# Kernel tuning notes

Hardware: AMD Instinct MI355X
Metric: run time of the kernel (lower is better)

Reference implementation:

```python
import jax, jax.numpy as jnp
import numpy as np

B, T, D, H = 32, 2048, 256, 512


def setup_inputs() -> dict:
    key = jax.random.key(0)
    k1, k2, k3, k4 = jax.random.split(key, 4)
    datamat = jax.random.normal(k1, (B, T, D), jnp.float32)
    datalens = jax.random.randint(k2, (B,), 0, T, jnp.int32)
    si = 1.0 / np.sqrt(D)
    sh = 1.0 / np.sqrt(H)
    # flax OptimizedLSTMCell: input dense has no bias, hidden dense has bias.
    Wi = jax.random.uniform(k3, (D, 4 * H), jnp.float32, -si, si)
    Wh = jax.random.uniform(k4, (H, 4 * H), jnp.float32, -sh, sh)
    b = jnp.zeros((4 * H,), jnp.float32)
    return {"datamat": datamat, "datalens": datalens, "Wi": Wi, "Wh": Wh, "b": b}


def _lstm(datamat, datalens, Wi, Wh, b):
    Bsz, Tlen, _ = datamat.shape
    Hd = Wh.shape[0]
    # Precompute input projection for all timesteps: [B,T,4H]
    x_proj = jnp.einsum('btd,dg->btg', datamat, Wi)
    c0 = jnp.zeros((Bsz, Hd), datamat.dtype)
    h0 = jnp.zeros((Bsz, Hd), datamat.dtype)

    def step(state, xg):
        c, h, lc, lh, t = state
        gates = xg + h @ Wh + b            # [B,4H], gate order i,f,g,o
        i, f, g, o = jnp.split(gates, 4, axis=-1)
        new_c = jax.nn.sigmoid(f) * c + jax.nn.sigmoid(i) * jnp.tanh(g)
        new_h = jax.nn.sigmoid(o) * jnp.tanh(new_c)
        # latch carry at the last valid step (t < seq_len), matching flax RNN
        # which selects the carry at index seq_len-1 from an unmasked scan.
        valid = (t < datalens)[:, None]
        lc = jnp.where(valid, new_c, lc)
        lh = jnp.where(valid, new_h, lh)
        return (new_c, new_h, lc, lh, t + 1), new_h

    init = (c0, h0, c0, h0, jnp.int32(0))
    (_, _, lc, lh, _), ys = jax.lax.scan(step, init, jnp.swapaxes(x_proj, 0, 1))
    return (lc, lh), jnp.swapaxes(ys, 0, 1)  # carry=(c,h), outputs [B,T,H]


def reference(datamat, datalens, Wi, Wh, b):
    return _lstm(datamat, datalens, Wi, Wh, b)
```

## Files before the change

kernel.cpp:

```cpp
#include <hip/hip_runtime.h>
#include <cstdint>

static constexpr int BATCH  = 32;
static constexpr int TLEN   = 2048;
static constexpr int DIN    = 256;
static constexpr int HDIM   = 512;
static constexpr int G4     = 2048;
static constexpr int NSLICE = 8;
static constexpr int HCB    = 64;
static constexpr int CPB    = 256;
static constexpr int NTHR   = 512;
static constexpr int NWAVE  = 8;
static constexpr int KL     = 96;
static constexpr int KL2    = 48;
static constexpr int NBLK   = BATCH * NSLICE;

typedef _Float16 h2v __attribute__((ext_vector_type(2)));
typedef uint32_t u32x4 __attribute__((ext_vector_type(4)));

__device__ __forceinline__ uint32_t pack_f16x2(float a, float b) {
    h2v v;
    v[0] = (_Float16)a;
    v[1] = (_Float16)b;
    return __builtin_bit_cast(uint32_t, v);
}

__device__ __forceinline__ float dot2f(uint32_t w, uint32_t u, float acc) {
#if __has_builtin(__builtin_amdgcn_fdot2)
    return __builtin_amdgcn_fdot2(__builtin_bit_cast(h2v, w),
                                  __builtin_bit_cast(h2v, u), acc, false);
#else
    h2v a = __builtin_bit_cast(h2v, w);
    h2v b = __builtin_bit_cast(h2v, u);
    return acc + (float)a[0] * (float)b[0] + (float)a[1] * (float)b[1];
#endif
}

__device__ __forceinline__ float sigmoidf_(float x) {
    return 1.0f / (1.0f + __expf(-x));
}
__device__ __forceinline__ float tanhf_(float x) {
    return 1.0f - 2.0f / (1.0f + __expf(2.0f * x));
}

__device__ __forceinline__ u32x4 load_agent_u128(const uint32_t* p) {
    u32x4 r;
    asm volatile("global_load_dwordx4 %0, %1, off sc0 sc1\n\t"
                 "s_waitcnt vmcnt(0)"
                 : "=&v"(r) : "v"(p) : "memory");
    return r;
}

__global__ __launch_bounds__(NTHR, 2)
__attribute__((amdgpu_waves_per_eu(2, 2)))
void lstm_persist(
    const float* __restrict__ x, const int* __restrict__ lens,
    const float* __restrict__ Wi, const float* __restrict__ Wh,
    const float* __restrict__ bias, float* __restrict__ out,
    uint32_t* __restrict__ hT)
{
    const int bid = blockIdx.x;
    const int xcd = bid & 7;
    const int t8  = bid >> 3;
    const int b   = xcd * 4 + (t8 & 3);
    const int s   = t8 >> 2;

    const int tid = threadIdx.x;
    const int w   = tid >> 6;
    const int l   = tid & 63;

    __shared__ __align__(16) uint32_t u_lds[NWAVE][KL2];
    __shared__ float gp[2][NWAVE][CPB];

    uint32_t wgt[4][KL2];
    #pragma unroll
    for (int q = 0; q < 4; ++q) {
        const int c    = 4 * l + q;
        const int gcol = (c >> 6) * HDIM + s * HCB + (c & 63);
        #pragma unroll
        for (int m = 0; m < KL2; ++m) {
            const int k0 = KL * w + 2 * m;
            const int k1 = k0 + 1;
            const float f0 = (k0 < DIN) ? Wi[(size_t)k0 * G4 + gcol]
                                        : Wh[(size_t)(k0 - DIN) * G4 + gcol];
            const float f1 = (k1 < DIN) ? Wi[(size_t)k1 * G4 + gcol]
                                        : Wh[(size_t)(k1 - DIN) * G4 + gcol];
            wgt[q][m] = pack_f16x2(f0, f1);
        }
    }

    float c_st = 0.f, lc_st = 0.f, lh_st = 0.f;
    float b_i = 0.f, b_f = 0.f, b_g = 0.f, b_o = 0.f;
    if (tid < HCB) {
        const int col = s * HCB + tid;
        b_i = bias[col];
        b_f = bias[HDIM + col];
        b_g = bias[2 * HDIM + col];
        b_o = bias[3 * HDIM + col];
    }
    const int len_b = lens[b];

    const float* xb = x + (size_t)b * TLEN * DIN;
    float* ys = out + 2 * BATCH * HDIM;

    const int  k0    = KL * w + 2 * l;
    const int  hk0   = KL * w + 4 * l;
    const bool is_x  = (l < KL2) && (k0 < DIN);
    const bool is_h4 = (l < KL2 / 2) && (hk0 >= DIN);

    float2 xx_cur = make_float2(0.f, 0.f);
    if (is_x) xx_cur = *(const float2*)(xb + k0);

    for (int t = 0; t < TLEN; ++t) {
        if (is_x) {
            u_lds[w][l] = pack_f16x2(xx_cur.x, xx_cur.y);
            if (t + 1 < TLEN)
                xx_cur = *(const float2*)(xb + (size_t)(t + 1) * DIN + k0);
        }
        if (is_h4) {
            const uint32_t* src =
                hT + (((size_t)(t & 1) * BATCH + b) * HDIM + (hk0 - DIN));
            const uint32_t tag = (uint32_t)t;
            u32x4 v;
            for (;;) {
                v = load_agent_u128(src);
                if ((v.x >> 16) == tag && (v.y >> 16) == tag &&
                    (v.z >> 16) == tag && (v.w >> 16) == tag) break;
            }
            uint2 pr;
            pr.x = (v.x & 0xFFFFu) | (v.y << 16);
            pr.y = (v.z & 0xFFFFu) | (v.w << 16);
            *(uint2*)&u_lds[w][2 * l] = pr;
        }

        float a0 = 0.f, a1 = 0.f, a2 = 0.f, a3 = 0.f;
        const uint4* uv = (const uint4*)&u_lds[w][0];
        #pragma unroll
        for (int m4 = 0; m4 < KL2 / 4; ++m4) {
            const uint4 uu = uv[m4];
            a0 = dot2f(wgt[0][4 * m4 + 0], uu.x, a0);
            a0 = dot2f(wgt[0][4 * m4 + 1], uu.y, a0);
            a0 = dot2f(wgt[0][4 * m4 + 2], uu.z, a0);
            a0 = dot2f(wgt[0][4 * m4 + 3], uu.w, a0);
            a1 = dot2f(wgt[1][4 * m4 + 0], uu.x, a1);
            a1 = dot2f(wgt[1][4 * m4 + 1], uu.y, a1);
            a1 = dot2f(wgt[1][4 * m4 + 2], uu.z, a1);
            a1 = dot2f(wgt[1][4 * m4 + 3], uu.w, a1);
            a2 = dot2f(wgt[2][4 * m4 + 0], uu.x, a2);
            a2 = dot2f(wgt[2][4 * m4 + 1], uu.y, a2);
            a2 = dot2f(wgt[2][4 * m4 + 2], uu.z, a2);
            a2 = dot2f(wgt[2][4 * m4 + 3], uu.w, a2);
            a3 = dot2f(wgt[3][4 * m4 + 0], uu.x, a3);
            a3 = dot2f(wgt[3][4 * m4 + 1], uu.y, a3);
            a3 = dot2f(wgt[3][4 * m4 + 2], uu.z, a3);
            a3 = dot2f(wgt[3][4 * m4 + 3], uu.w, a3);
        }
        float4 av;
        av.x = a0; av.y = a1; av.z = a2; av.w = a3;
        *(float4*)&gp[t & 1][w][4 * l] = av;

        __syncthreads();

        if (tid < HCB) {
            float si = b_i, sf = b_f, sg = b_g, so = b_o;
            #pragma unroll
            for (int ww = 0; ww < NWAVE; ++ww) {
                si += gp[t & 1][ww][tid];
                sf += gp[t & 1][ww][HCB + tid];
                sg += gp[t & 1][ww][2 * HCB + tid];
                so += gp[t & 1][ww][3 * HCB + tid];
            }
            const float ig = sigmoidf_(si);
            const float fg = sigmoidf_(sf);
            const float gg = tanhf_(sg);
            const float og = sigmoidf_(so);
            const float cn = fg * c_st + ig * gg;
            const float hn = og * tanhf_(cn);
            c_st = cn;
            if (t < len_b) { lc_st = cn; lh_st = hn; }
            const _Float16 hf = (_Float16)hn;
            const uint32_t word = ((uint32_t)(t + 1) << 16) |
                                  (uint32_t)__builtin_bit_cast(uint16_t, hf);
            __hip_atomic_store(
                &hT[((size_t)((t + 1) & 1) * BATCH + b) * HDIM + s * HCB + tid],
                word, __ATOMIC_RELAXED, __HIP_MEMORY_SCOPE_AGENT);
            ys[((size_t)b * TLEN + t) * HDIM + s * HCB + tid] = hn;
        }
    }

    if (tid < HCB) {
        out[(size_t)b * HDIM + s * HCB + tid] = lc_st;
        out[BATCH * HDIM + (size_t)b * HDIM + s * HCB + tid] = lh_st;
    }
}

extern "C" void kernel_launch(void* const* d_in, const int* in_sizes, int n_in,
                              void* d_out, int out_size, void* d_ws, size_t ws_size,
                              hipStream_t stream)
{
    const float* x    = (const float*)d_in[0];
    const int*   lens = (const int*)d_in[1];
    const float* Wi   = (const float*)d_in[2];
    const float* Wh   = (const float*)d_in[3];
    const float* bias = (const float*)d_in[4];
    float* out = (float*)d_out;

    uint32_t* hT = (uint32_t*)d_ws;
    const size_t init_bytes = (size_t)2 * BATCH * HDIM * sizeof(uint32_t);
    hipMemsetAsync(d_ws, 0, init_bytes, stream);

    hipLaunchKernelGGL(lstm_persist, dim3(NBLK), dim3(NTHR), 0, stream,
                       x, lens, Wi, Wh, bias, out, hT);
}
```

Before: 4.009 ms.

## Poll hidden state with a single wave and broadcast via LDS flag

Instead of several waves each spin-polling a slice of the previous hidden state from global memory, wave 7 alone polls the full 512-element h vector with wide loads, packs it into LDS and publishes readiness through an LDS flag that waves 2-6 spin on. This cuts the number of concurrent global polling requests per block and the cross-wave polling traffic on the recurrent critical path. The trade-off is an extra intra-block LDS spin and a serialization point on one wave. It also drops the waves_per_eu attribute and moves the latch update after the hidden-state store.

```diff
diff --git a/kernel.cpp b/kernel.cpp
--- a/kernel.cpp
+++ b/kernel.cpp
@@ -13,6 +13,7 @@
 static constexpr int NWAVE  = 8;
 static constexpr int KL     = 96;
 static constexpr int KL2    = 48;
+static constexpr int KWORDS = 384;
 static constexpr int NBLK   = BATCH * NSLICE;
 
 typedef _Float16 h2v __attribute__((ext_vector_type(2)));
@@ -51,9 +52,7 @@
     return r;
 }
 
-__global__ __launch_bounds__(NTHR, 2)
-__attribute__((amdgpu_waves_per_eu(2, 2)))
-void lstm_persist(
+__global__ __launch_bounds__(NTHR, 2) void lstm_persist(
     const float* __restrict__ x, const int* __restrict__ lens,
     const float* __restrict__ Wi, const float* __restrict__ Wh,
     const float* __restrict__ bias, float* __restrict__ out,
@@ -69,8 +68,9 @@
     const int w   = tid >> 6;
     const int l   = tid & 63;
 
-    __shared__ __align__(16) uint32_t u_lds[NWAVE][KL2];
+    __shared__ __align__(16) uint32_t u_lds[KWORDS];
     __shared__ float gp[2][NWAVE][CPB];
+    __shared__ uint32_t hflag;
 
     uint32_t wgt[4][KL2];
     #pragma unroll
@@ -89,6 +89,9 @@
         }
     }
 
+    if (tid == 0) hflag = 0xFFFFFFFFu;
+    __syncthreads();
+
     float c_st = 0.f, lc_st = 0.f, lh_st = 0.f;
     float b_i = 0.f, b_f = 0.f, b_g = 0.f, b_o = 0.f;
     if (tid < HCB) {
@@ -103,38 +106,52 @@
     const float* xb = x + (size_t)b * TLEN * DIN;
     float* ys = out + 2 * BATCH * HDIM;
 
-    const int  k0    = KL * w + 2 * l;
-    const int  hk0   = KL * w + 4 * l;
-    const bool is_x  = (l < KL2) && (k0 < DIN);
-    const bool is_h4 = (l < KL2 / 2) && (hk0 >= DIN);
+    const int  k0   = KL * w + 2 * l;
+    const bool is_x = (l < KL2) && (k0 < DIN);
 
     float2 xx_cur = make_float2(0.f, 0.f);
     if (is_x) xx_cur = *(const float2*)(xb + k0);
 
     for (int t = 0; t < TLEN; ++t) {
+        const uint32_t tag = (uint32_t)t;
         if (is_x) {
-            u_lds[w][l] = pack_f16x2(xx_cur.x, xx_cur.y);
+            u_lds[48 * w + l] = pack_f16x2(xx_cur.x, xx_cur.y);
             if (t + 1 < TLEN)
                 xx_cur = *(const float2*)(xb + (size_t)(t + 1) * DIN + k0);
         }
-        if (is_h4) {
-            const uint32_t* src =
-                hT + (((size_t)(t & 1) * BATCH + b) * HDIM + (hk0 - DIN));
-            const uint32_t tag = (uint32_t)t;
-            u32x4 v;
+        if (w == 7) {
+            const uint32_t* slab =
+                hT + (((size_t)(t & 1) * BATCH + b) * HDIM + 8 * l);
             for (;;) {
-                v = load_agent_u128(src);
-                if ((v.x >> 16) == tag && (v.y >> 16) == tag &&
-                    (v.z >> 16) == tag && (v.w >> 16) == tag) break;
+                const u32x4 va = load_agent_u128(slab);
+                const u32x4 vb = load_agent_u128(slab + 4);
+                const bool ok =
+                    (va.x >> 16) == tag && (va.y >> 16) == tag &&
+                    (va.z >> 16) == tag && (va.w >> 16) == tag &&
+                    (vb.x >> 16) == tag && (vb.y >> 16) == tag &&
+                    (vb.z >> 16) == tag && (vb.w >> 16) == tag;
+                if (__all(ok)) {
+                    uint4 pk;
+                    pk.x = (va.x & 0xFFFFu) | (va.y << 16);
+                    pk.y = (va.z & 0xFFFFu) | (va.w << 16);
+                    pk.z = (vb.x & 0xFFFFu) | (vb.y << 16);
+                    pk.w = (vb.z & 0xFFFFu) | (vb.w << 16);
+                    *(uint4*)&u_lds[128 + 4 * l] = pk;
+                    break;
+                }
             }
-            uint2 pr;
-            pr.x = (v.x & 0xFFFFu) | (v.y << 16);
-            pr.y = (v.z & 0xFFFFu) | (v.w << 16);
-            *(uint2*)&u_lds[w][2 * l] = pr;
+            asm volatile("s_waitcnt lgkmcnt(0)" ::: "memory");
+            if (l == 0)
+                __hip_atomic_store(&hflag, tag, __ATOMIC_RELAXED,
+                                   __HIP_MEMORY_SCOPE_WORKGROUP);
+        } else if (w >= 2) {
+            while (__hip_atomic_load(&hflag, __ATOMIC_RELAXED,
+                                     __HIP_MEMORY_SCOPE_WORKGROUP) != tag) {}
+            asm volatile("" ::: "memory");
         }
 
         float a0 = 0.f, a1 = 0.f, a2 = 0.f, a3 = 0.f;
-        const uint4* uv = (const uint4*)&u_lds[w][0];
+        const uint4* uv = (const uint4*)&u_lds[48 * w];
         #pragma unroll
         for (int m4 = 0; m4 < KL2 / 4; ++m4) {
             const uint4 uu = uv[m4];
@@ -177,7 +194,6 @@
             const float cn = fg * c_st + ig * gg;
             const float hn = og * tanhf_(cn);
             c_st = cn;
-            if (t < len_b) { lc_st = cn; lh_st = hn; }
             const _Float16 hf = (_Float16)hn;
             const uint32_t word = ((uint32_t)(t + 1) << 16) |
                                   (uint32_t)__builtin_bit_cast(uint16_t, hf);
@@ -185,6 +201,7 @@
                 &hT[((size_t)((t + 1) & 1) * BATCH + b) * HDIM + s * HCB + tid],
                 word, __ATOMIC_RELAXED, __HIP_MEMORY_SCOPE_AGENT);
             ys[((size_t)b * TLEN + t) * HDIM + s * HCB + tid] = hn;
+            if (t < len_b) { lc_st = cn; lh_st = hn; }
         }
     }
 
```

After: 4.810 ms. +20.0%, slower.
